# Kernel optimization log

Hardware: AMD Instinct MI355X
Metric: run time of the kernel (lower is better)

The kernel has to match this reference:

```python
import jax, jax.numpy as jnp
import numpy as np

B, M, N = 16, 64, 64
F = 64
H2 = 2 * F
L = 2
OUT1, OUT2, PREDS = 32, 32, 256


def skew(x):
    # (b,m,n,c) -> (b,m,m+n-1,c); row i shifted right by i
    b, m, n, c = x.shape
    pad = jnp.pad(x, ((0, 0), (0, 0), (0, m - 1), (0, 0)))
    return jax.vmap(lambda row, r: jnp.roll(row, r, axis=1), in_axes=(1, 0), out_axes=1)(pad, jnp.arange(m))


def unskew(x):
    b, m, n2, c = x.shape
    n = n2 - m + 1
    un = jax.vmap(lambda row, r: jnp.roll(row, -r, axis=1), in_axes=(1, 0), out_axes=1)(x, jnp.arange(m))
    return un[:, :, :n]


def _ln(x, s, b, eps=1e-6):
    mu = jnp.mean(x, axis=-1, keepdims=True)
    var = jnp.mean(jnp.square(x - mu), axis=-1, keepdims=True)
    return (x - mu) * jax.lax.rsqrt(var + eps) * s + b


def _diag_layer(xin, lns, lnb, wis, bis, wss, bss, woc, boc, h0p):
    # xin: (b,m,n2,2F); scan over diagonals (n2 axis)
    b, m, n2, h2 = xin.shape
    f = h2 // 2

    def step(carry, xt):  # xt: (b,m,2F)
        h, c = carry
        xn = _ln(xt, lns, lnb)
        # is_kernel: 1x1 conv == linear; ss_kernel: causal k=2 conv along m
        hprev = jnp.pad(h, ((0, 0), (1, 0), (0, 0)))[:, :-1]
        z = xn @ wis + bis + hprev @ wss[0] + h @ wss[1] + bss  # (b,m,4F)
        fg, ig, og, gg = jnp.split(z, 4, axis=-1)
        cn = jax.nn.sigmoid(fg) * c + jax.nn.sigmoid(ig) * jnp.tanh(gg)
        hn = jax.nn.sigmoid(og) * jnp.tanh(cn)
        x_out = hn @ woc + boc + xn  # residual uses post-LN x (as in source)
        return (hn, cn), x_out

    h0t = jnp.broadcast_to(h0p, (b, m, f))  # h0p: (1,F)
    c0 = jnp.zeros((b, m, f), xin.dtype)
    _, out = jax.lax.scan(step, (h0t, c0), xin.transpose(2, 0, 1, 3))
    return out.transpose(1, 2, 0, 3)


def _forward(im, conv_in_k, conv_in_b, ln_s, ln_b, w_is, b_is, w_ss, b_ss,
             w_oc, b_oc, h0, w_out1, b_out1, w_out2, b_out2, w_head, b_head):
    # mask-A for the 7x7 input conv
    mask = jnp.ones(conv_in_k.shape, conv_in_k.dtype)
    mask = mask.at[3:, 4:].set(0.0)
    mask = mask.at[4:].set(0.0)
    mask = mask.at[3, 3].set(0.0)
    x = skew(im)  # (b,m,n2,1)
    x = jax.lax.conv_general_dilated(x, conv_in_k * mask, (1, 1), 'SAME',
                                     dimension_numbers=('NHWC', 'HWIO', 'NHWC')) + conv_in_b
    b, m, n2, h2 = x.shape
    for l in range(ln_s.shape[0]):
        left = _diag_layer(x, ln_s[l, 0], ln_b[l, 0], w_is[l, 0], b_is[l, 0],
                           w_ss[l, 0], b_ss[l, 0], w_oc[l, 0], b_oc[l, 0], h0[l, 0])
        right = _diag_layer(x[:, :, ::-1, :], ln_s[l, 1], ln_b[l, 1], w_is[l, 1], b_is[l, 1],
                            w_ss[l, 1], b_ss[l, 1], w_oc[l, 1], b_oc[l, 1], h0[l, 1])[:, :, ::-1, :]
        right = jnp.concatenate([jnp.zeros((b, 1, n2, h2), x.dtype), right[:, :-1]], axis=1)
        x = left + right
    x = unskew(x)  # (b,m,n,2F)
    x = x @ w_out1 + b_out1
    x = x @ w_out2 + b_out2
    return x @ w_head + b_head  # (b,m,n,256)


def setup_inputs() -> dict:
    key = jax.random.key(0)
    ks = jax.random.split(key, 10)
    rn = lambda k, s: jax.random.normal(k, s, jnp.float32) * 0.05
    return {
        "im": jax.random.uniform(ks[0], (B, M, N, 1), jnp.float32),
        "conv_in_k": rn(ks[1], (7, 7, 1, H2)),
        "conv_in_b": jnp.zeros((H2,), jnp.float32),
        "ln_s": jnp.ones((L, 2, H2), jnp.float32),
        "ln_b": jnp.zeros((L, 2, H2), jnp.float32),
        "w_is": rn(ks[2], (L, 2, H2, 4 * F)),
        "b_is": jnp.zeros((L, 2, 4 * F), jnp.float32),
        "w_ss": rn(ks[3], (L, 2, 2, F, 4 * F)),
        "b_ss": jnp.zeros((L, 2, 4 * F), jnp.float32),
        "w_oc": rn(ks[4], (L, 2, F, H2)),
        "b_oc": jnp.zeros((L, 2, H2), jnp.float32),
        "h0": rn(ks[5], (L, 2, 1, F)),
        "w_out1": rn(ks[6], (H2, OUT1)),
        "b_out1": jnp.zeros((OUT1,), jnp.float32),
        "w_out2": rn(ks[7], (OUT1, OUT2)),
        "b_out2": jnp.zeros((OUT2,), jnp.float32),
        "w_head": rn(ks[8], (OUT2, PREDS)),
        "b_head": jnp.zeros((PREDS,), jnp.float32),
    }


def reference(im, conv_in_k, conv_in_b, ln_s, ln_b, w_is, b_is, w_ss, b_ss,
              w_oc, b_oc, h0, w_out1, b_out1, w_out2, b_out2, w_head, b_head):
    return _forward(im, conv_in_k, conv_in_b, ln_s, ln_b, w_is, b_is, w_ss, b_ss,
                    w_oc, b_oc, h0, w_out1, b_out1, w_out2, b_out2, w_head, b_head)
```

## Files before the change

kernel.cpp:

```cpp
#include <hip/hip_runtime.h>

typedef unsigned short ushort_t;
typedef unsigned int uint_t;
typedef __attribute__((ext_vector_type(8))) short s8bf;
typedef __attribute__((ext_vector_type(4))) float f32x4;

#define N2 127
#define ACT ((size_t)16*64*127*128)
#define HNE ((size_t)16*64*127*64)
#define MBW ((size_t)32*3*127*64)

__device__ inline float bf_lo(uint_t v){ return __uint_as_float(v << 16); }
__device__ inline float bf_hi(uint_t v){ return __uint_as_float(v & 0xffff0000u); }
__device__ inline ushort_t f2bf(float f){
  uint_t u = __float_as_uint(f);
  uint_t r = ((u >> 16) & 1u) + 0x7fffu;
  return (ushort_t)((u + r) >> 16);
}
__device__ inline uint_t cvt_pk_bf16(float lo, float hi){
  uint_t r;
  asm("v_cvt_pk_bf16_f32 %0, %1, %2" : "=v"(r) : "v"(lo), "v"(hi));
  return r;
}
__device__ inline float bf2f(ushort_t h){ return __uint_as_float(((uint_t)h) << 16); }
__device__ inline float frcp(float x){ return __builtin_amdgcn_rcpf(x); }
__device__ inline float sigm(float x){ return frcp(1.f + __expf(-x)); }
__device__ inline float tanhf_(float x){
  float e = __expf(2.f * x);
  return 1.f - 2.f * frcp(1.f + e);
}
__device__ inline void unpack8(uint4 u, float* x){
  x[0]=bf_lo(u.x); x[1]=bf_hi(u.x); x[2]=bf_lo(u.y); x[3]=bf_hi(u.y);
  x[4]=bf_lo(u.z); x[5]=bf_hi(u.z); x[6]=bf_lo(u.w); x[7]=bf_hi(u.w);
}
__device__ inline f32x4 zero4(){ f32x4 v; v[0]=0.f; v[1]=0.f; v[2]=0.f; v[3]=0.f; return v; }
__device__ inline f32x4 splat4(float s){ f32x4 v; v[0]=s; v[1]=s; v[2]=s; v[3]=s; return v; }

__device__ inline void rowstats(const float* xr, float& mu, float& rstd){
  float s0=0.f, q0=0.f;
#pragma unroll
  for (int k = 0; k < 32; k++){ s0 += xr[k]; q0 += xr[k]*xr[k]; }
  s0 += __shfl_xor(s0, 1); q0 += __shfl_xor(q0, 1);
  s0 += __shfl_xor(s0, 2); q0 += __shfl_xor(q0, 2);
  mu = s0 * 0.0078125f;
  float var = q0 * 0.0078125f - mu*mu;
  rstd = rsqrtf(var + 1e-6f);
}

__global__ void pack_kernel(const float* __restrict__ w_is, const float* __restrict__ w_ss,
                            const float* __restrict__ b_is, const float* __restrict__ b_ss,
                            const float* __restrict__ w_oc, const float* __restrict__ w1,
                            const float* __restrict__ w2, const float* __restrict__ wh,
                            const float* __restrict__ ck,
                            ushort_t* __restrict__ zWp, ushort_t* __restrict__ wisp,
                            ushort_t* __restrict__ wocp,
                            float* __restrict__ zbias, float* __restrict__ w1T,
                            float* __restrict__ w2T, float* __restrict__ whT,
                            float* __restrict__ kw, uint_t* __restrict__ mb)
{
  int idx = blockIdx.x * 256 + threadIdx.x;
  if (idx < 131072){
    int ld = idx >> 15; int r = idx & 32767;
    int e = r & 7, lane = (r >> 3) & 63, ctg = (r >> 9) & 15, kk = r >> 13;
    int k = kk*32 + ((lane >> 4) & 3)*8 + e;
    int n = ctg*16 + (lane & 15);
    float v;
    if (k < 64) v = w_ss[(((size_t)ld*2 + 0)*64 + k)*256 + n];
    else        v = w_ss[(((size_t)ld*2 + 1)*64 + (k-64))*256 + n];
    zWp[idx] = f2bf(v);
  } else if (idx < 262144){
    int r0 = idx - 131072;
    int ld = r0 >> 15; int r = r0 & 32767;
    int e = r & 7, lane = (r >> 3) & 63, ctg = (r >> 9) & 15, kk = r >> 13;
    int k = kk*32 + ((lane >> 4) & 3)*8 + e;
    int n = ctg*16 + (lane & 15);
    wisp[r0] = f2bf(w_is[((size_t)ld*128 + k)*256 + n]);
  } else if (idx < 294912){
    int r0 = idx - 262144;
    int ld = r0 >> 13; int r = r0 & 8191;
    int e = r & 7, lane = (r >> 3) & 63, ctg = (r >> 9) & 7, kk = (r >> 12) & 1;
    int k = kk*32 + ((lane >> 4) & 3)*8 + e;
    int n = ctg*16 + (lane & 15);
    wocp[r0] = f2bf(w_oc[((size_t)ld*64 + k)*128 + n]);
  } else if (idx < 295936){
    int r = idx - 294912;
    zbias[r] = b_is[r] + b_ss[r];
  } else if (idx < 300032){
    int r = idx - 295936;
    int c = r >> 7, k = r & 127;
    w1T[r] = w1[k*32 + c];
  } else if (idx < 301056){
    int r = idx - 300032;
    int c = r >> 5, k = r & 31;
    w2T[r] = w2[k*32 + c];
  } else if (idx < 309248){
    int r = idx - 301056;
    int o = r >> 5, k = r & 31;
    whT[r] = wh[k*256 + o];
  } else if (idx < 312320){
    int r = idx - 309248;
    int tau = r >> 7, ch = r & 127;
    int di, dj;
    if (tau < 21){ di = tau/7 - 3; dj = tau%7 - 3; } else { di = 0; dj = tau - 24; }
    kw[r] = ck[((di+3)*7 + (dj+3))*128 + ch];
  } else if (idx < (int)(312320 + MBW)){
    mb[idx - 312320] = 0u;
  }
}

__global__ __launch_bounds__(256) void conv_kernel(const float* __restrict__ im,
                const float* __restrict__ cb, const float* __restrict__ kw,
                ushort_t* __restrict__ out)
{
  __shared__ float ims[4][64];
  const int tid = threadIdx.x;
  const int b = blockIdx.x >> 6;
  const int i = blockIdx.x & 63;
  {
    int r = tid >> 6, c = tid & 63;
    int ii = i - 3 + r;
    ims[r][c] = (ii >= 0) ? im[(b*64 + ii)*64 + c] : 0.f;
  }
  const int ch = tid & 127;
  const int jh = tid >> 7;
  float kwreg[24];
#pragma unroll
  for (int tau = 0; tau < 24; tau++) kwreg[tau] = kw[tau*128 + ch];
  const float cbv = cb[ch];
  __syncthreads();
  ushort_t* orow = out + ((size_t)(b*64 + i)*N2)*128 + ch;
#pragma unroll 1
  for (int jt = 0; jt < 64; jt++){
    int j = jt*2 + jh;
    if (j >= N2) break;
    int base = j - i;
    float acc = cbv;
#pragma unroll
    for (int tau = 0; tau < 24; tau++){
      int di = (tau < 21) ? (tau/7 - 3) : 0;
      int dj = (tau < 21) ? (tau%7 - 3) : (tau - 24);
      int jx = base + dj - di;
      int r = di + 3;
      if (jx >= 0 && jx < 64)
        acc += ims[r][jx] * kwreg[tau];
    }
    orow[(size_t)j*128] = f2bf(acc);
  }
}

__device__ inline void write_frags(const ushort_t* __restrict__ XN,
                                   ushort_t* __restrict__ dst, int tid){
  int lane = tid & 63, kkq = tid >> 6;
  int quad = (lane >> 4) & 3, l16 = lane & 15;
#pragma unroll
  for (int rt = 0; rt < 4; rt++){
    uint4 v = *(const uint4*)&XN[(size_t)(rt*16 + l16)*136 + kkq*32 + quad*8];
    *(uint4*)(dst + (size_t)((kkq*4 + rt)*64 + lane)*8) = v;
  }
}

__device__ inline void ln_to_XN(ushort_t* __restrict__ XN, int row, int lq,
                                const float* xr, float mu, float rstd,
                                const float* __restrict__ ln_s,
                                const float* __restrict__ ln_b, int ld){
  uint_t o[16];
#pragma unroll
  for (int k2 = 0; k2 < 16; k2++){
    int c = lq*32 + 2*k2;
    float a = (xr[2*k2]   - mu)*rstd*ln_s[ld*128 + c]     + ln_b[ld*128 + c];
    float b = (xr[2*k2+1] - mu)*rstd*ln_s[ld*128 + c + 1] + ln_b[ld*128 + c + 1];
    o[k2] = cvt_pk_bf16(a, b);
  }
  uint4* dst = (uint4*)&XN[(size_t)row*136 + lq*32];
#pragma unroll
  for (int q = 0; q < 4; q++) dst[q] = make_uint4(o[q*4], o[q*4+1], o[q*4+2], o[q*4+3]);
}

__global__ __launch_bounds__(256) void stage0_kernel(
    int lnlyr, const ushort_t* __restrict__ Xbuf,
    const float* __restrict__ ln_s, const float* __restrict__ ln_b,
    ushort_t* __restrict__ xnfL, ushort_t* __restrict__ xnfR)
{
  __shared__ __align__(16) ushort_t XN[64*136];

  const int tid = threadIdx.x;
  const int bj = blockIdx.x;
  const int b = bj / 127, j = bj - b*127;
  const int row = tid >> 2, lq = tid & 3;

  float xr[32];
  {
    const uint4* p = (const uint4*)(Xbuf + ((size_t)(b*64 + row)*N2 + j)*128 + lq*32);
    unpack8(p[0], xr); unpack8(p[1], xr+8); unpack8(p[2], xr+16); unpack8(p[3], xr+24);
  }
  float mu, rstd;
  rowstats(xr, mu, rstd);

  ln_to_XN(XN, row, lq, xr, mu, rstd, ln_s, ln_b, lnlyr*2 + 0);
  __syncthreads();
  write_frags(XN, xnfL + (size_t)bj*8192, tid);
  __syncthreads();
  ln_to_XN(XN, row, lq, xr, mu, rstd, ln_s, ln_b, lnlyr*2 + 1);
  __syncthreads();
  write_frags(XN, xnfR + (size_t)bj*8192, tid);
}

__global__ __launch_bounds__(256, 2) void stage12_kernel(
    int mode, int woclyr, int lnlyr,
    ushort_t* __restrict__ Xbuf,
    const ushort_t* __restrict__ hnL, const ushort_t* __restrict__ hnR,
    const ushort_t* __restrict__ wocp, const float* __restrict__ b_oc,
    const float* __restrict__ ln_s, const float* __restrict__ ln_b,
    ushort_t* __restrict__ xnfL, ushort_t* __restrict__ xnfR)
{
  __shared__ __align__(16) float Xout[64*132];
  __shared__ __align__(16) ushort_t XN[64*136];

  const int tid = threadIdx.x;
  const int bj = blockIdx.x;
  const int b = bj / 127, j = bj - b*127;
  const int w = tid >> 6, lane = tid & 63, quad = (lane >> 4) & 3, l16 = lane & 15;
  const int row = tid >> 2, lq = tid & 3;

  float xr[32];
  {
    const uint4* p = (const uint4*)(Xbuf + ((size_t)(b*64 + row)*N2 + j)*128 + lq*32);
    unpack8(p[0], xr); unpack8(p[1], xr+8); unpack8(p[2], xr+16); unpack8(p[3], xr+24);
  }
  float mu, rstd;
  rowstats(xr, mu, rstd);

#pragma unroll 1
  for (int s = 0; s < 2; s++){
    const int ld = woclyr*2 + s;
    const ushort_t* hp = s ? hnR : hnL;
    s8bf ha[2][4];
#pragma unroll
    for (int kk = 0; kk < 2; kk++)
#pragma unroll
      for (int rt = 0; rt < 4; rt++)
        ha[kk][rt] = *(const s8bf*)(hp +
            ((size_t)(b*64 + rt*16 + l16)*N2 + j)*64 + kk*32 + quad*8);
    ln_to_XN(XN, row, lq, xr, mu, rstd, ln_s, ln_b, ld);
    __syncthreads();
    s8bf bw[2][2];
#pragma unroll
    for (int kk = 0; kk < 2; kk++)
#pragma unroll
      for (int jt = 0; jt < 2; jt++)
        bw[kk][jt] = *(const s8bf*)(wocp + (size_t)ld*8192 + (size_t)(((kk*8 + (2*w + jt))*64 + lane)*8));
    f32x4 a2[4][2];
#pragma unroll
    for (int rt = 0; rt < 4; rt++){ a2[rt][0] = zero4(); a2[rt][1] = zero4(); }
#pragma unroll
    for (int kk = 0; kk < 2; kk++)
#pragma unroll
      for (int rt = 0; rt < 4; rt++){
#pragma unroll
        for (int jt = 0; jt < 2; jt++)
          a2[rt][jt] = __builtin_amdgcn_mfma_f32_16x16x32_bf16(ha[kk][rt], bw[kk][jt], a2[rt][jt], 0, 0, 0);
      }
    const float bv0 = b_oc[ld*128 + 32*w + l16];
    const float bv1 = b_oc[ld*128 + 32*w + 16 + l16];
#pragma unroll
    for (int rt = 0; rt < 4; rt++)
#pragma unroll
      for (int jt = 0; jt < 2; jt++){
        int col = 32*w + 16*jt + l16;
        float bv = jt ? bv1 : bv0;
#pragma unroll
        for (int r = 0; r < 4; r++){
          int rr = rt*16 + quad*4 + r;
          float v = a2[rt][jt][r] + bv + bf2f(XN[(size_t)rr*136 + col]);
          if (s == 0) Xout[(size_t)rr*132 + col] = v;
          else if (rr < 63) Xout[(size_t)(rr + 1)*132 + col] += v;
        }
      }
    __syncthreads();
  }

  float xo[32];
#pragma unroll
  for (int k = 0; k < 32; k++) xo[k] = Xout[(size_t)row*132 + lq*32 + k];
  {
    uint_t o[16];
#pragma unroll
    for (int k = 0; k < 16; k++) o[k] = cvt_pk_bf16(xo[2*k], xo[2*k + 1]);
    uint4* dst = (uint4*)(Xbuf + ((size_t)(b*64 + row)*N2 + j)*128 + lq*32);
#pragma unroll
    for (int q2 = 0; q2 < 4; q2++) dst[q2] = make_uint4(o[q2*4], o[q2*4+1], o[q2*4+2], o[q2*4+3]);
  }
  if (mode == 2) return;

  float mu2, rstd2;
  rowstats(xo, mu2, rstd2);
  ln_to_XN(XN, row, lq, xo, mu2, rstd2, ln_s, ln_b, lnlyr*2 + 0);
  __syncthreads();
  write_frags(XN, xnfL + (size_t)bj*8192, tid);
  __syncthreads();
  ln_to_XN(XN, row, lq, xo, mu2, rstd2, ln_s, ln_b, lnlyr*2 + 1);
  __syncthreads();
  write_frags(XN, xnfR + (size_t)bj*8192, tid);
}

__global__ __launch_bounds__(256, 1) void diag_kernel(
    const ushort_t* __restrict__ xnfL, const ushort_t* __restrict__ xnfR,
    ushort_t* __restrict__ hnL, ushort_t* __restrict__ hnR,
    const ushort_t* __restrict__ zWp, const ushort_t* __restrict__ wisp,
    const float* __restrict__ zbias, const float* __restrict__ h0, int layer,
    uint_t* __restrict__ mb)
{
  __shared__ ushort_t A[2][16][136];

  const int tid = threadIdx.x;
  const int g = blockIdx.x & 3;
  const int b = (blockIdx.x >> 2) & 15;
  const int d = blockIdx.x >> 6;
  const int ld = layer*2 + d;
  const ushort_t* xnf = d ? xnfR : xnfL;
  ushort_t* hp = d ? hnR : hnL;

  const int w = tid >> 6;
  const int lane = tid & 63;
  const int quad = lane >> 4;
  const int l16 = lane & 15;
  const int cg = w*16 + l16;

  s8bf bss[4][4], bis[4][4];
#pragma unroll
  for (int kk = 0; kk < 4; kk++)
#pragma unroll
    for (int ct = 0; ct < 4; ct++){
      size_t fo = (size_t)(((kk*16 + (w + 4*ct))*64 + lane)*8);
      bss[kk][ct] = *(const s8bf*)(zWp  + (size_t)ld*32768 + fo);
      bis[kk][ct] = *(const s8bf*)(wisp + (size_t)ld*32768 + fo);
    }
  float zb[4];
#pragma unroll
  for (int ct = 0; ct < 4; ct++) zb[ct] = zbias[ld*256 + ct*64 + cg];

  float c_reg[4] = {0.f, 0.f, 0.f, 0.f};

  {
    int r2 = tid >> 4, q8 = tid & 15;
    const float* h0p = h0 + ld*64;
#pragma unroll
    for (int k = 0; k < 8; k++){
      int c = q8*8 + k;
      ushort_t hb = f2bf(h0p[c & 63]);
      ushort_t v;
      if (c < 64) v = (g == 0 && r2 == 0) ? (ushort_t)0 : hb;
      else        v = hb;
      A[0][r2][c] = v;
      A[1][r2][c] = v;
    }
  }

  const int stp8 = d ? -8192 : 8192;
  const ushort_t* xbase = xnf + ((size_t)b*127 + (d ? 126 : 0))*8192;
  uint4 xf[4];
#pragma unroll
  for (int kk = 0; kk < 4; kk++)
    xf[kk] = *(const uint4*)(xbase + (size_t)((kk*4 + g)*64 + lane)*8);

  f32x4 acc[4];
#pragma unroll
  for (int ct = 0; ct < 4; ct++) acc[ct] = splat4(zb[ct]);
#pragma unroll
  for (int kk = 0; kk < 4; kk++){
    s8bf a = *(const s8bf*)&xf[kk];
#pragma unroll
    for (int ct = 0; ct < 4; ct++)
      acc[ct] = __builtin_amdgcn_mfma_f32_16x16x32_bf16(a, bis[kk][ct], acc[ct], 0, 0, 0);
  }
  const ushort_t* pfp = xbase + stp8;
#pragma unroll
  for (int kk = 0; kk < 4; kk++)
    xf[kk] = *(const uint4*)(pfp + (size_t)((kk*4 + g)*64 + lane)*8);
  pfp += stp8;

  const int dj64 = d ? -64 : 64;
  ushort_t* hlane = hp + ((size_t)(b*64 + g*16 + quad*4)*N2 + (d ? 126 : 0))*64 + cg;

  const int bd = b*2 + d;
  uint_t* mbOut = mb + ((size_t)(bd*3 + g)*127)*64;
  const uint_t* mbIn = mb + ((size_t)(bd*3 + (g > 0 ? g - 1 : 0))*127)*64;
  const uint_t stampBase = (uint_t)layer * 127u;
  const bool isProd = (g < 3);
  const bool isCons = (g > 0) && (w == 1);

  __syncthreads();

#pragma unroll 1
  for (int t = 0; t < 127; t++){
    const int pr = t & 1, pn = pr ^ 1;
    const uint_t stamp = stampBase + (uint_t)t + 1u;
    const bool doFetch = isCons && (t < 126);

    uint_t pv = 0;
    if (doFetch)
      pv = __hip_atomic_load(mbIn + (size_t)t*64 + lane,
                             __ATOMIC_RELAXED, __HIP_MEMORY_SCOPE_AGENT);

#pragma unroll
    for (int kk = 0; kk < 4; kk++){
      s8bf af = *(const s8bf*)&A[pr][l16][kk*32 + quad*8];
#pragma unroll
      for (int ct = 0; ct < 4; ct++)
        acc[ct] = __builtin_amdgcn_mfma_f32_16x16x32_bf16(af, bss[kk][ct], acc[ct], 0, 0, 0);
    }

#pragma unroll
    for (int r = 0; r < 4; r++){
      float fg = sigm(acc[0][r]);
      float ig = sigm(acc[1][r]);
      float og = sigm(acc[2][r]);
      float gg = tanhf_(acc[3][r]);
      float cn = fg*c_reg[r] + ig*gg;
      c_reg[r] = cn;
      float hn = og * tanhf_(cn);
      int rr = quad*4 + r;
      ushort_t hb = f2bf(hn);
      A[pn][rr][64 + cg] = hb;
      if (rr < 15) A[pn][rr + 1][cg] = hb;
      hlane[(size_t)r*8128] = hb;
      if (r == 3 && isProd && quad == 3 && t < 126)
        __hip_atomic_store(mbOut + (size_t)t*64 + cg,
                           (stamp << 16) | (uint_t)hb,
                           __ATOMIC_RELAXED, __HIP_MEMORY_SCOPE_AGENT);
    }
    hlane += dj64;

    if (t < 126){
#pragma unroll
      for (int ct = 0; ct < 4; ct++) acc[ct] = splat4(zb[ct]);
#pragma unroll
      for (int kk = 0; kk < 4; kk++){
        s8bf a = *(const s8bf*)&xf[kk];
#pragma unroll
        for (int ct = 0; ct < 4; ct++)
          acc[ct] = __builtin_amdgcn_mfma_f32_16x16x32_bf16(a, bis[kk][ct], acc[ct], 0, 0, 0);
      }
      if (t < 125){
#pragma unroll
        for (int kk = 0; kk < 4; kk++)
          xf[kk] = *(const uint4*)(pfp + (size_t)((kk*4 + g)*64 + lane)*8);
        pfp += stp8;
      }
    }

    if (doFetch){
      while (!__all((pv >> 16) == stamp))
        pv = __hip_atomic_load(mbIn + (size_t)t*64 + lane,
                               __ATOMIC_RELAXED, __HIP_MEMORY_SCOPE_AGENT);
      A[pn][0][lane] = (ushort_t)(pv & 0xffffu);
    }

    __syncthreads();
  }
}

__global__ __launch_bounds__(256) void head_kernel(
    const ushort_t* __restrict__ xfin,
    const float* __restrict__ w1T, const float* __restrict__ b1,
    const float* __restrict__ w2T, const float* __restrict__ b2,
    const float* __restrict__ whT, const float* __restrict__ bh,
    float* __restrict__ out)
{
  __shared__ float xf[64][132];
  __shared__ float v1[64][36];
  __shared__ float v2[64][36];
  int tid = threadIdx.x;
  int b = blockIdx.x >> 6, i = blockIdx.x & 63;
  {
    int jj = tid >> 2, q = tid & 3;
    size_t base = ((size_t)(b*64 + i)*N2 + (i + jj))*128 + q*32;
    const uint4* pL = (const uint4*)(xfin + base);
    float x[32];
    unpack8(pL[0], x); unpack8(pL[1], x+8); unpack8(pL[2], x+16); unpack8(pL[3], x+24);
#pragma unroll
    for (int k = 0; k < 32; k++) xf[jj][q*32 + k] = x[k];
  }
  __syncthreads();
  {
    int c1 = tid & 31, jg = tid >> 5;
    float accv[8];
#pragma unroll
    for (int q = 0; q < 8; q++) accv[q] = b1[c1];
#pragma unroll 1
    for (int kc = 0; kc < 4; kc++){
      float wr[32];
      const float4* wp = (const float4*)(w1T + c1*128 + kc*32);
#pragma unroll
      for (int kk = 0; kk < 8; kk++) ((float4*)wr)[kk] = wp[kk];
#pragma unroll
      for (int jj2 = 0; jj2 < 8; jj2++){
        int jr = jg*8 + jj2;
        float a0=0.f,a1=0.f,a2=0.f,a3=0.f;
#pragma unroll
        for (int kk = 0; kk < 8; kk++){
          float4 xv = *(const float4*)&xf[jr][kc*32 + kk*4];
          a0 += xv.x*wr[kk*4]; a1 += xv.y*wr[kk*4+1]; a2 += xv.z*wr[kk*4+2]; a3 += xv.w*wr[kk*4+3];
        }
        accv[jj2] += (a0+a1)+(a2+a3);
      }
    }
#pragma unroll
    for (int jj2 = 0; jj2 < 8; jj2++) v1[jg*8 + jj2][c1] = accv[jj2];
  }
  __syncthreads();
  {
    int c2 = tid & 31, jg = tid >> 5;
    float wr[32];
    const float4* wp = (const float4*)(w2T + c2*32);
#pragma unroll
    for (int kk = 0; kk < 8; kk++) ((float4*)wr)[kk] = wp[kk];
#pragma unroll 1
    for (int jj2 = 0; jj2 < 8; jj2++){
      int jr = jg*8 + jj2;
      float a0=0.f,a1=0.f,a2=0.f,a3=0.f;
#pragma unroll
      for (int kk = 0; kk < 8; kk++){
        float4 xv = *(const float4*)&v1[jr][kk*4];
        a0 += xv.x*wr[kk*4]; a1 += xv.y*wr[kk*4+1]; a2 += xv.z*wr[kk*4+2]; a3 += xv.w*wr[kk*4+3];
      }
      v2[jr][c2] = b2[c2] + (a0+a1)+(a2+a3);
    }
  }
  __syncthreads();
  {
    int o = tid;
    float wr[32];
    const float4* wp = (const float4*)(whT + o*32);
#pragma unroll
    for (int kk = 0; kk < 8; kk++) ((float4*)wr)[kk] = wp[kk];
    float bo = bh[o];
#pragma unroll 1
    for (int jr = 0; jr < 64; jr++){
      float a0=0.f,a1=0.f,a2=0.f,a3=0.f;
#pragma unroll
      for (int kk = 0; kk < 8; kk++){
        float4 xv = *(const float4*)&v2[jr][kk*4];
        a0 += xv.x*wr[kk*4]; a1 += xv.y*wr[kk*4+1]; a2 += xv.z*wr[kk*4+2]; a3 += xv.w*wr[kk*4+3];
      }
      out[(((size_t)b*64 + i)*64 + jr)*256 + o] = bo + (a0+a1)+(a2+a3);
    }
  }
}

extern "C" void kernel_launch(void* const* d_in, const int* in_sizes, int n_in,
                              void* d_out, int out_size, void* d_ws, size_t ws_size,
                              hipStream_t stream)
{
  const float* im   = (const float*)d_in[0];
  const float* ck   = (const float*)d_in[1];
  const float* cb   = (const float*)d_in[2];
  const float* ln_s = (const float*)d_in[3];
  const float* ln_b = (const float*)d_in[4];
  const float* w_is = (const float*)d_in[5];
  const float* b_is = (const float*)d_in[6];
  const float* w_ss = (const float*)d_in[7];
  const float* b_ss = (const float*)d_in[8];
  const float* w_oc = (const float*)d_in[9];
  const float* b_oc = (const float*)d_in[10];
  const float* h0   = (const float*)d_in[11];
  const float* w1   = (const float*)d_in[12];
  const float* b1   = (const float*)d_in[13];
  const float* w2   = (const float*)d_in[14];
  const float* b2   = (const float*)d_in[15];
  const float* wh   = (const float*)d_in[16];
  const float* bh   = (const float*)d_in[17];

  ushort_t* Xbuf = (ushort_t*)d_ws;
  ushort_t* xnfL = Xbuf + ACT;
  ushort_t* xnfR = xnfL + ACT;
  ushort_t* hnL  = xnfR + ACT;
  ushort_t* hnR  = hnL + HNE;
  ushort_t* zWp  = hnR + HNE;
  ushort_t* wisp = zWp + 131072;
  ushort_t* wocp = wisp + 131072;
  float* zbias = (float*)(wocp + 32768);
  float* w1T   = zbias + 1024;
  float* w2T   = w1T + 4096;
  float* whT   = w2T + 1024;
  float* kw    = whT + 8192;
  uint_t* mb   = (uint_t*)d_out;

  pack_kernel<<<4268, 256, 0, stream>>>(w_is, w_ss, b_is, b_ss, w_oc, w1, w2, wh, ck,
                                        zWp, wisp, wocp, zbias, w1T, w2T, whT, kw, mb);
  conv_kernel<<<1024, 256, 0, stream>>>(im, cb, kw, Xbuf);
  stage0_kernel<<<2032, 256, 0, stream>>>(0, Xbuf, ln_s, ln_b, xnfL, xnfR);
  diag_kernel<<<128, 256, 0, stream>>>(xnfL, xnfR, hnL, hnR, zWp, wisp, zbias, h0, 0, mb);
  stage12_kernel<<<2032, 256, 0, stream>>>(1, 0, 1, Xbuf, hnL, hnR,
                                           wocp, b_oc, ln_s, ln_b, xnfL, xnfR);
  diag_kernel<<<128, 256, 0, stream>>>(xnfL, xnfR, hnL, hnR, zWp, wisp, zbias, h0, 1, mb);
  stage12_kernel<<<2032, 256, 0, stream>>>(2, 1, 0, Xbuf, hnL, hnR,
                                           wocp, b_oc, ln_s, ln_b, xnfL, xnfR);
  head_kernel<<<1024, 256, 0, stream>>>(Xbuf, w1T, b1, w2T, b2, whT, bh, (float*)d_out);
}
```

Measured before the change: 752.4 us.

## Widen stage12 kernel to 512 threads and stage hidden state through LDS

```diff
diff --git a/kernel.cpp b/kernel.cpp
--- a/kernel.cpp
+++ b/kernel.cpp
@@ -42,6 +42,18 @@
   for (int k = 0; k < 32; k++){ s0 += xr[k]; q0 += xr[k]*xr[k]; }
   s0 += __shfl_xor(s0, 1); q0 += __shfl_xor(q0, 1);
   s0 += __shfl_xor(s0, 2); q0 += __shfl_xor(q0, 2);
+  mu = s0 * 0.0078125f;
+  float var = q0 * 0.0078125f - mu*mu;
+  rstd = rsqrtf(var + 1e-6f);
+}
+
+__device__ inline void rowstats16(const float* xr, float& mu, float& rstd){
+  float s0=0.f, q0=0.f;
+#pragma unroll
+  for (int k = 0; k < 16; k++){ s0 += xr[k]; q0 += xr[k]*xr[k]; }
+  s0 += __shfl_xor(s0, 1); q0 += __shfl_xor(q0, 1);
+  s0 += __shfl_xor(s0, 2); q0 += __shfl_xor(q0, 2);
+  s0 += __shfl_xor(s0, 4); q0 += __shfl_xor(q0, 4);
   mu = s0 * 0.0078125f;
   float var = q0 * 0.0078125f - mu*mu;
   rstd = rsqrtf(var + 1e-6f);
@@ -159,6 +171,19 @@
   }
 }
 
+__device__ inline void write_frags512(const ushort_t* __restrict__ XN,
+                                      ushort_t* __restrict__ dst, int tid){
+  int lane = tid & 63, t8 = tid >> 6;
+  int quad = (lane >> 4) & 3, l16 = lane & 15;
+  int kk = t8 >> 1, rh = (t8 & 1)*2;
+#pragma unroll
+  for (int i = 0; i < 2; i++){
+    int rt = rh + i;
+    uint4 v = *(const uint4*)&XN[(size_t)(rt*16 + l16)*136 + kk*32 + quad*8];
+    *(uint4*)(dst + (size_t)((kk*4 + rt)*64 + lane)*8) = v;
+  }
+}
+
 __device__ inline void ln_to_XN(ushort_t* __restrict__ XN, int row, int lq,
                                 const float* xr, float mu, float rstd,
                                 const float* __restrict__ ln_s,
@@ -174,6 +199,23 @@
   uint4* dst = (uint4*)&XN[(size_t)row*136 + lq*32];
 #pragma unroll
   for (int q = 0; q < 4; q++) dst[q] = make_uint4(o[q*4], o[q*4+1], o[q*4+2], o[q*4+3]);
+}
+
+__device__ inline void ln_to_XN16(ushort_t* __restrict__ XN, int row, int lq,
+                                  const float* xr, float mu, float rstd,
+                                  const float* __restrict__ ln_s,
+                                  const float* __restrict__ ln_b, int ld){
+  uint_t o[8];
+#pragma unroll
+  for (int k2 = 0; k2 < 8; k2++){
+    int c = lq*16 + 2*k2;
+    float a = (xr[2*k2]   - mu)*rstd*ln_s[ld*128 + c]     + ln_b[ld*128 + c];
+    float b = (xr[2*k2+1] - mu)*rstd*ln_s[ld*128 + c + 1] + ln_b[ld*128 + c + 1];
+    o[k2] = cvt_pk_bf16(a, b);
+  }
+  uint4* dst = (uint4*)&XN[(size_t)row*136 + lq*16];
+  dst[0] = make_uint4(o[0], o[1], o[2], o[3]);
+  dst[1] = make_uint4(o[4], o[5], o[6], o[7]);
 }
 
 __global__ __launch_bounds__(256) void stage0_kernel(
@@ -205,7 +247,7 @@
   write_frags(XN, xnfR + (size_t)bj*8192, tid);
 }
 
-__global__ __launch_bounds__(256, 2) void stage12_kernel(
+__global__ __launch_bounds__(512, 1) void stage12_kernel(
     int mode, int woclyr, int lnlyr,
     ushort_t* __restrict__ Xbuf,
     const ushort_t* __restrict__ hnL, const ushort_t* __restrict__ hnR,
@@ -215,92 +257,83 @@
 {
   __shared__ __align__(16) float Xout[64*132];
   __shared__ __align__(16) ushort_t XN[64*136];
+  __shared__ __align__(16) ushort_t XNh[64*72];
 
   const int tid = threadIdx.x;
   const int bj = blockIdx.x;
   const int b = bj / 127, j = bj - b*127;
-  const int w = tid >> 6, lane = tid & 63, quad = (lane >> 4) & 3, l16 = lane & 15;
-  const int row = tid >> 2, lq = tid & 3;
-
-  float xr[32];
-  {
-    const uint4* p = (const uint4*)(Xbuf + ((size_t)(b*64 + row)*N2 + j)*128 + lq*32);
-    unpack8(p[0], xr); unpack8(p[1], xr+8); unpack8(p[2], xr+16); unpack8(p[3], xr+24);
+  const int w8 = tid >> 6;
+  const int lane = tid & 63, quad = (lane >> 4) & 3, l16 = lane & 15;
+  const int row = tid >> 3, lq = tid & 7;
+
+  float xr[16];
+  {
+    const uint4* p = (const uint4*)(Xbuf + ((size_t)(b*64 + row)*N2 + j)*128 + lq*16);
+    unpack8(p[0], xr); unpack8(p[1], xr+8);
   }
   float mu, rstd;
-  rowstats(xr, mu, rstd);
+  rowstats16(xr, mu, rstd);
 
 #pragma unroll 1
   for (int s = 0; s < 2; s++){
     const int ld = woclyr*2 + s;
-    const ushort_t* hp = s ? hnR : hnL;
-    s8bf ha[2][4];
+    ln_to_XN16(XN, row, lq, xr, mu, rstd, ln_s, ln_b, ld);
+    {
+      const ushort_t* hp = s ? hnR : hnL;
+      const uint4* p = (const uint4*)(hp + ((size_t)(b*64 + row)*N2 + j)*64 + lq*8);
+      *(uint4*)&XNh[(size_t)row*72 + lq*8] = p[0];
+    }
+    __syncthreads();
+    s8bf bw[2];
 #pragma unroll
     for (int kk = 0; kk < 2; kk++)
-#pragma unroll
-      for (int rt = 0; rt < 4; rt++)
-        ha[kk][rt] = *(const s8bf*)(hp +
-            ((size_t)(b*64 + rt*16 + l16)*N2 + j)*64 + kk*32 + quad*8);
-    ln_to_XN(XN, row, lq, xr, mu, rstd, ln_s, ln_b, ld);
-    __syncthreads();
-    s8bf bw[2][2];
+      bw[kk] = *(const s8bf*)(wocp + (size_t)ld*8192 + (size_t)(((kk*8 + w8)*64 + lane)*8));
+    f32x4 a2[4];
+#pragma unroll
+    for (int rt = 0; rt < 4; rt++) a2[rt] = zero4();
 #pragma unroll
     for (int kk = 0; kk < 2; kk++)
 #pragma unroll
-      for (int jt = 0; jt < 2; jt++)
-        bw[kk][jt] = *(const s8bf*)(wocp + (size_t)ld*8192 + (size_t)(((kk*8 + (2*w + jt))*64 + lane)*8));
-    f32x4 a2[4][2];
-#pragma unroll
-    for (int rt = 0; rt < 4; rt++){ a2[rt][0] = zero4(); a2[rt][1] = zero4(); }
-#pragma unroll
-    for (int kk = 0; kk < 2; kk++)
-#pragma unroll
       for (int rt = 0; rt < 4; rt++){
-#pragma unroll
-        for (int jt = 0; jt < 2; jt++)
-          a2[rt][jt] = __builtin_amdgcn_mfma_f32_16x16x32_bf16(ha[kk][rt], bw[kk][jt], a2[rt][jt], 0, 0, 0);
+        s8bf a = *(const s8bf*)&XNh[(size_t)(rt*16 + l16)*72 + kk*32 + quad*8];
+        a2[rt] = __builtin_amdgcn_mfma_f32_16x16x32_bf16(a, bw[kk], a2[rt], 0, 0, 0);
       }
-    const float bv0 = b_oc[ld*128 + 32*w + l16];
-    const float bv1 = b_oc[ld*128 + 32*w + 16 + l16];
+    const float bv = b_oc[ld*128 + w8*16 + l16];
+    const int col = w8*16 + l16;
 #pragma unroll
     for (int rt = 0; rt < 4; rt++)
 #pragma unroll
-      for (int jt = 0; jt < 2; jt++){
-        int col = 32*w + 16*jt + l16;
-        float bv = jt ? bv1 : bv0;
-#pragma unroll
-        for (int r = 0; r < 4; r++){
-          int rr = rt*16 + quad*4 + r;
-          float v = a2[rt][jt][r] + bv + bf2f(XN[(size_t)rr*136 + col]);
-          if (s == 0) Xout[(size_t)rr*132 + col] = v;
-          else if (rr < 63) Xout[(size_t)(rr + 1)*132 + col] += v;
-        }
+      for (int r = 0; r < 4; r++){
+        int rr = rt*16 + quad*4 + r;
+        float v = a2[rt][r] + bv + bf2f(XN[(size_t)rr*136 + col]);
+        if (s == 0) Xout[(size_t)rr*132 + col] = v;
+        else if (rr < 63) Xout[(size_t)(rr + 1)*132 + col] += v;
       }
     __syncthreads();
   }
 
-  float xo[32];
-#pragma unroll
-  for (int k = 0; k < 32; k++) xo[k] = Xout[(size_t)row*132 + lq*32 + k];
-  {
-    uint_t o[16];
-#pragma unroll
-    for (int k = 0; k < 16; k++) o[k] = cvt_pk_bf16(xo[2*k], xo[2*k + 1]);
-    uint4* dst = (uint4*)(Xbuf + ((size_t)(b*64 + row)*N2 + j)*128 + lq*32);
-#pragma unroll
-    for (int q2 = 0; q2 < 4; q2++) dst[q2] = make_uint4(o[q2*4], o[q2*4+1], o[q2*4+2], o[q2*4+3]);
+  float xo[16];
+#pragma unroll
+  for (int k = 0; k < 16; k++) xo[k] = Xout[(size_t)row*132 + lq*16 + k];
+  {
+    uint_t o[8];
+#pragma unroll
+    for (int k = 0; k < 8; k++) o[k] = cvt_pk_bf16(xo[2*k], xo[2*k + 1]);
+    uint4* dst = (uint4*)(Xbuf + ((size_t)(b*64 + row)*N2 + j)*128 + lq*16);
+    dst[0] = make_uint4(o[0], o[1], o[2], o[3]);
+    dst[1] = make_uint4(o[4], o[5], o[6], o[7]);
   }
   if (mode == 2) return;
 
   float mu2, rstd2;
-  rowstats(xo, mu2, rstd2);
-  ln_to_XN(XN, row, lq, xo, mu2, rstd2, ln_s, ln_b, lnlyr*2 + 0);
-  __syncthreads();
-  write_frags(XN, xnfL + (size_t)bj*8192, tid);
-  __syncthreads();
-  ln_to_XN(XN, row, lq, xo, mu2, rstd2, ln_s, ln_b, lnlyr*2 + 1);
-  __syncthreads();
-  write_frags(XN, xnfR + (size_t)bj*8192, tid);
+  rowstats16(xo, mu2, rstd2);
+  ln_to_XN16(XN, row, lq, xo, mu2, rstd2, ln_s, ln_b, lnlyr*2 + 0);
+  __syncthreads();
+  write_frags512(XN, xnfL + (size_t)bj*8192, tid);
+  __syncthreads();
+  ln_to_XN16(XN, row, lq, xo, mu2, rstd2, ln_s, ln_b, lnlyr*2 + 1);
+  __syncthreads();
+  write_frags512(XN, xnfR + (size_t)bj*8192, tid);
 }
 
 __global__ __launch_bounds__(256, 1) void diag_kernel(
@@ -591,10 +624,10 @@
   conv_kernel<<<1024, 256, 0, stream>>>(im, cb, kw, Xbuf);
   stage0_kernel<<<2032, 256, 0, stream>>>(0, Xbuf, ln_s, ln_b, xnfL, xnfR);
   diag_kernel<<<128, 256, 0, stream>>>(xnfL, xnfR, hnL, hnR, zWp, wisp, zbias, h0, 0, mb);
-  stage12_kernel<<<2032, 256, 0, stream>>>(1, 0, 1, Xbuf, hnL, hnR,
+  stage12_kernel<<<2032, 512, 0, stream>>>(1, 0, 1, Xbuf, hnL, hnR,
                                            wocp, b_oc, ln_s, ln_b, xnfL, xnfR);
   diag_kernel<<<128, 256, 0, stream>>>(xnfL, xnfR, hnL, hnR, zWp, wisp, zbias, h0, 1, mb);
-  stage12_kernel<<<2032, 256, 0, stream>>>(2, 1, 0, Xbuf, hnL, hnR,
+  stage12_kernel<<<2032, 512, 0, stream>>>(2, 1, 0, Xbuf, hnL, hnR,
                                            wocp, b_oc, ln_s, ln_b, xnfL, xnfR);
   head_kernel<<<1024, 256, 0, stream>>>(Xbuf, w1T, b1, w2T, b2, whT, bh, (float*)d_out);
 }
```

New measurement: 668.8 us. -11.1%, faster.
